# Kernel tuning notes

Hardware: AMD Instinct MI355X
Metric: run time of the kernel (lower is better)

## Reference

```python
import jax, jax.numpy as jnp
import numpy as np

POWERS = (0, 1, 2)
IN_F, OUT_F = 64, 64
B, N, T = 8, 2048, 12


def setup_inputs() -> dict:
    key = jax.random.key(0)
    ks = jax.random.split(key, 8)
    inp = {
        "x": jax.random.normal(ks[0], (B, IN_F, N, T), dtype=jnp.float32),
        "adj": jax.random.uniform(ks[1], (B, N, N), dtype=jnp.float32),
    }
    # Xavier-uniform weights per adjacency power, zero biases (as in initialize_weights)
    limit = float(np.sqrt(6.0 / (IN_F + OUT_F)))
    for i, p in enumerate(POWERS):
        inp[f"W{p}"] = jax.random.uniform(ks[2 + i], (IN_F, OUT_F), jnp.float32, -limit, limit)
        inp[f"b{p}"] = jnp.zeros((OUT_F,), jnp.float32)
    return inp


def _gcn_conv(x, adj, W, b, a_power):
    # x: [B, F, N, T]; W: [F, O]; adj: [B, N, N]
    h = jnp.einsum('bfnt,fo->bont', x, W) + b[None, :, None, None]
    # repeated diffusion along node axis: h[f, n] <- sum_m adj[n, m] h[f, m]
    for _ in range(a_power):
        h = jnp.einsum('bnm,bomt->bont', adj, h)
    return jax.nn.leaky_relu(h)  # default negative_slope 0.01, same as torch


def reference(x, adj, W0, b0, W1, b1, W2, b2):
    params = {0: (W0, b0), 1: (W1, b1), 2: (W2, b2)}
    outs = [_gcn_conv(x, adj, params[p][0], params[p][1], p) for p in POWERS]
    return jnp.concatenate(outs, axis=1)  # [B, len(POWERS)*O, N, T]
```

## Files before the change

kernel.cpp:

```cpp
#include <hip/hip_runtime.h>

#define B_ 8
#define N_ 2048
#define T_ 12
#define F_ 64
#define NT 24576
#define CH 192
#define C_ 768

typedef __bf16 bf16x8 __attribute__((ext_vector_type(8)));
typedef float f32x4 __attribute__((ext_vector_type(4)));

typedef const __attribute__((address_space(1))) unsigned int as1_uint;
typedef __attribute__((address_space(3))) unsigned int as3_uint;

__device__ __forceinline__ void gload16(const void* g, void* l) {
  __builtin_amdgcn_global_load_lds((as1_uint*)g, (as3_uint*)l, 16, 0, 0);
}

__device__ __forceinline__ unsigned short f2bf(float f) {
  unsigned int u = __float_as_uint(f);
  u += 0x7FFFu + ((u >> 16) & 1u);
  return (unsigned short)(u >> 16);
}

__device__ __forceinline__ float leaky(float v) {
  return v >= 0.0f ? v : 0.01f * v;
}

__global__ __launch_bounds__(256) void convert_adj_k(const float* __restrict__ adj,
                                                     unsigned short* __restrict__ adjb) {
  size_t i = (size_t)blockIdx.x * 256 + threadIdx.x;
  const float4 v = reinterpret_cast<const float4*>(adj)[i];
  ushort4 u;
  u.x = f2bf(v.x); u.y = f2bf(v.y); u.z = f2bf(v.z); u.w = f2bf(v.w);
  reinterpret_cast<ushort4*>(adjb)[i] = u;
}

__device__ __forceinline__ void stage_wt(const float* __restrict__ W,
                                         unsigned short* Wt, int tid) {
  const int f = tid >> 2;
  const int q = tid & 3;
  const float4* row = reinterpret_cast<const float4*>(W + f * 64 + q * 16);
#pragma unroll
  for (int v4 = 0; v4 < 4; ++v4) {
    float4 v = row[v4];
    const int ob = q * 16 + v4 * 4;
    Wt[(ob + 0) * 72 + f] = f2bf(v.x);
    Wt[(ob + 1) * 72 + f] = f2bf(v.y);
    Wt[(ob + 2) * 72 + f] = f2bf(v.z);
    Wt[(ob + 3) * 72 + f] = f2bf(v.w);
  }
}

__global__ __launch_bounds__(256) void p0_k(const float* __restrict__ x,
                                            const float* __restrict__ W0,
                                            const float* __restrict__ bia0,
                                            float* __restrict__ out) {
  __shared__ unsigned short Wt[64 * 72];
  __shared__ float bias[64];
  const int tid = threadIdx.x;
  stage_wt(W0, Wt, tid);
  if (tid < 64) bias[tid] = bia0[tid];
  __syncthreads();

  const int lane = tid & 63;
  const int wave = tid >> 6;
  const int b = blockIdx.y;
  const int e = blockIdx.x * 64 + wave * 16 + (lane & 15);
  const int fgrp = (lane >> 4) * 8;
  const float* xb = x + (size_t)b * F_ * NT;

  bf16x8 xf[2];
#pragma unroll
  for (int kf = 0; kf < 2; ++kf)
#pragma unroll
    for (int j = 0; j < 8; ++j)
      xf[kf][j] = (__bf16)xb[(size_t)(fgrp + kf * 32 + j) * NT + e];

  float* outb = out + (size_t)b * CH * NT;
#pragma unroll
  for (int ob = 0; ob < 4; ++ob) {
    f32x4 acc = {};
#pragma unroll
    for (int kf = 0; kf < 2; ++kf) {
      bf16x8 af = *reinterpret_cast<const bf16x8*>(
          &Wt[(ob * 16 + (lane & 15)) * 72 + kf * 32 + fgrp]);
      acc = __builtin_amdgcn_mfma_f32_16x16x32_bf16(af, xf[kf], acc, 0, 0, 0);
    }
#pragma unroll
    for (int r = 0; r < 4; ++r) {
      const int o = ob * 16 + (lane >> 4) * 4 + r;
      outb[(size_t)o * NT + e] = leaky(acc[r] + bias[o]);
    }
  }
}

__global__ __launch_bounds__(256) void p12_k(const float* __restrict__ x,
                                             const float* __restrict__ W1,
                                             const float* __restrict__ bia1,
                                             const float* __restrict__ W2,
                                             const float* __restrict__ bia2,
                                             unsigned short* __restrict__ G1,
                                             unsigned short* __restrict__ G2) {
  __shared__ unsigned short Wt[2][64 * 72];
  __shared__ float bias[2][64];
  const int tid = threadIdx.x;
  stage_wt(W1, Wt[0], tid);
  stage_wt(W2, Wt[1], tid);
  if (tid < 64) bias[0][tid] = bia1[tid];
  else if (tid < 128) bias[1][tid - 64] = bia2[tid - 64];
  __syncthreads();

  const int lane = tid & 63;
  const int wave = tid >> 6;
  const int b = blockIdx.y;
  const int n = blockIdx.x * 16 + (lane & 15);
  const int fgrp = (lane >> 4) * 8;
  const float* xb = x + (size_t)b * F_ * NT;
  unsigned short* Gp[2] = {G1 + (size_t)b * C_ * N_, G2 + (size_t)b * C_ * N_};

#pragma unroll
  for (int it = 0; it < 3; ++it) {
    const int t = wave * 3 + it;
    const int e = n * T_ + t;

    bf16x8 xf[2];
#pragma unroll
    for (int kf = 0; kf < 2; ++kf)
#pragma unroll
      for (int j = 0; j < 8; ++j)
        xf[kf][j] = (__bf16)xb[(size_t)(fgrp + kf * 32 + j) * NT + e];

#pragma unroll
    for (int p = 0; p < 2; ++p) {
#pragma unroll
      for (int ob = 0; ob < 4; ++ob) {
        f32x4 acc = {};
#pragma unroll
        for (int kf = 0; kf < 2; ++kf) {
          bf16x8 af = *reinterpret_cast<const bf16x8*>(
              &Wt[p][(ob * 16 + (lane & 15)) * 72 + kf * 32 + fgrp]);
          acc = __builtin_amdgcn_mfma_f32_16x16x32_bf16(af, xf[kf], acc, 0, 0, 0);
        }
#pragma unroll
        for (int r = 0; r < 4; ++r) {
          const int o = ob * 16 + (lane >> 4) * 4 + r;
          Gp[p][(size_t)(o * T_ + t) * N_ + n] = f2bf(acc[r] + bias[p][o]);
        }
      }
    }
  }
}

__global__ __launch_bounds__(512, 2) void gemm8_k(
    const unsigned short* __restrict__ adjb,
    const unsigned short* __restrict__ Bt,
    float* __restrict__ out,
    unsigned short* __restrict__ Ht,
    const int mode, const int ochan_base)
{
  extern __shared__ __align__(16) unsigned short lds[];

  const int tid  = threadIdx.x;
  const int lane = tid & 63;
  const int wave = tid >> 6;
  const int wr = wave >> 2;
  const int wc = wave & 3;

  const int b  = blockIdx.x & 7;
  const int w  = blockIdx.x >> 3;
  const int n0 = (w & 7) * 256;
  const int c0 = (w >> 3) * 192;

  const unsigned short* A  = adjb + (size_t)b * N_ * N_;
  const unsigned short* Bm = Bt   + (size_t)b * C_ * N_;

  const int swzSrc = ((lane & 3) ^ ((lane >> 3) & 3)) * 8;
  const unsigned short* aSt1 = A + (size_t)(n0 + wave * 16 + (lane >> 2)) * N_ + swzSrc;
  const unsigned short* aSt2 = aSt1 + (size_t)128 * N_;
  const unsigned short* bSt1 = Bm + (size_t)(c0 + wave * 16 + (lane >> 2)) * N_ + swzSrc;
  const int brow2 = c0 + 128 + wave * 16 + (lane >> 2);
  const unsigned short* bSt2 = Bm + (size_t)(brow2 < C_ ? brow2 : C_ - 1) * N_ + swzSrc;
  const int ldsW = wave * 512;

  const int kg  = (lane >> 4) ^ ((lane >> 1) & 3);
  const int aRd = (wr * 128 + (lane & 15)) * 32 + kg * 8;
  const int bRd = (wc * 48  + (lane & 15)) * 32 + kg * 8;

  f32x4 acc[8][3] = {};
  bf16x8 afr[8], bfr[3];

#define STGA(LDSB, KT, KH) \
  gload16(aSt1 + (KT) * 64 + (KH) * 32, lds + (LDSB) + (KH) * 8192 + ldsW); \
  gload16(aSt2 + (KT) * 64 + (KH) * 32, lds + (LDSB) + (KH) * 8192 + ldsW + 4096);

#define STGB(LDSB, KT, KH) \
  gload16(bSt1 + (KT) * 64 + (KH) * 32, lds + (LDSB) + (KH) * 8192 + ldsW); \
  gload16(bSt2 + (KT) * 64 + (KH) * 32, lds + (LDSB) + (KH) * 8192 + ldsW + 4096);

#define RD_B(BUFB, KH) { \
  _Pragma("unroll") \
  for (int nf = 0; nf < 3; ++nf) \
    bfr[nf] = *(const bf16x8*)(lds + (BUFB) + (KH) * 8192 + nf * 512 + bRd); }

#define RD_A8(BUFA, KH) { \
  _Pragma("unroll") \
  for (int mm = 0; mm < 8; ++mm) \
    afr[mm] = *(const bf16x8*)(lds + (BUFA) + (KH) * 8192 + mm * 512 + aRd); }

#define MFMA24() { \
  _Pragma("unroll") \
  for (int mm = 0; mm < 8; ++mm) \
  _Pragma("unroll") \
  for (int nf = 0; nf < 3; ++nf) \
    acc[mm][nf] = __builtin_amdgcn_mfma_f32_16x16x32_bf16( \
        afr[mm], bfr[nf], acc[mm][nf], 0, 0, 0); }

#define MIDBAR() \
  __builtin_amdgcn_s_barrier(); \
  __builtin_amdgcn_s_setprio(1);

#define ENDBAR() \
  __builtin_amdgcn_s_setprio(0); \
  __builtin_amdgcn_s_barrier();

#define WAITV_(N) asm volatile("s_waitcnt vmcnt(" #N ")" ::: "memory");
#define WAITV(N) WAITV_(N)

  STGA(0, 0, 0)      STGB(32768, 0, 0)
  STGA(0, 0, 1)      STGB(32768, 0, 1)
  STGA(16384, 1, 0)  STGB(49152, 1, 0)
  WAITV(8)
  __builtin_amdgcn_s_barrier();

#pragma unroll 1
  for (int it = 0; it < 15; ++it) {
    const int kt0 = 2 * it;
    RD_B(32768, 0) RD_A8(0, 0)
    STGA(16384, kt0 + 1, 1) STGB(49152, kt0 + 1, 1)
    WAITV(8)
    MIDBAR() MFMA24() ENDBAR()
    RD_B(32768, 1) RD_A8(0, 1)
    STGA(0, kt0 + 2, 0) STGB(32768, kt0 + 2, 0)
    WAITV(8)
    MIDBAR() MFMA24() ENDBAR()
    RD_B(49152, 0) RD_A8(16384, 0)
    STGA(0, kt0 + 2, 1) STGB(32768, kt0 + 2, 1)
    WAITV(8)
    MIDBAR() MFMA24() ENDBAR()
    RD_B(49152, 1) RD_A8(16384, 1)
    STGA(16384, kt0 + 3, 0) STGB(49152, kt0 + 3, 0)
    WAITV(8)
    MIDBAR() MFMA24() ENDBAR()
  }

  {
    RD_B(32768, 0) RD_A8(0, 0)
    STGA(16384, 31, 1) STGB(49152, 31, 1)
    WAITV(8)
    MIDBAR() MFMA24() ENDBAR()
    RD_B(32768, 1) RD_A8(0, 1)
    WAITV(4)
    MIDBAR() MFMA24() ENDBAR()
    RD_B(49152, 0) RD_A8(16384, 0)
    WAITV(0)
    MIDBAR() MFMA24() ENDBAR()
    RD_B(49152, 1) RD_A8(16384, 1)
    MIDBAR() MFMA24()
    __builtin_amdgcn_s_setprio(0);
  }

  const int r4 = (lane >> 4) * 4;
  if (mode == 0) {
    float* outb = out + (size_t)b * CH * NT;
#pragma unroll
    for (int m = 0; m < 8; ++m) {
#pragma unroll
      for (int nf = 0; nf < 3; ++nf) {
        const int c = c0 + wc * 48 + nf * 16 + (lane & 15);
        const int o = c / 12;
        const int t = c - o * 12;
#pragma unroll
        for (int r = 0; r < 4; ++r) {
          const int n = n0 + wr * 128 + m * 16 + r4 + r;
          outb[((size_t)(ochan_base + o) * N_ + n) * T_ + t] = leaky(acc[m][nf][r]);
        }
      }
    }
  } else {
    unsigned short* Hb = Ht + (size_t)b * C_ * N_;
#pragma unroll
    for (int m = 0; m < 8; ++m) {
#pragma unroll
      for (int nf = 0; nf < 3; ++nf) {
        const int c = c0 + wc * 48 + nf * 16 + (lane & 15);
        const int nb = n0 + wr * 128 + m * 16 + r4;
        ushort4 u;
        u.x = f2bf(acc[m][nf][0]);
        u.y = f2bf(acc[m][nf][1]);
        u.z = f2bf(acc[m][nf][2]);
        u.w = f2bf(acc[m][nf][3]);
        *reinterpret_cast<ushort4*>(&Hb[(size_t)c * N_ + nb]) = u;
      }
    }
  }
#undef STGA
#undef STGB
#undef RD_B
#undef RD_A8
#undef MFMA24
#undef MIDBAR
#undef ENDBAR
#undef WAITV
#undef WAITV_
}

extern "C" void kernel_launch(void* const* d_in, const int* in_sizes, int n_in,
                              void* d_out, int out_size, void* d_ws, size_t ws_size,
                              hipStream_t stream) {
  const float* x   = (const float*)d_in[0];
  const float* adj = (const float*)d_in[1];
  const float* W0  = (const float*)d_in[2];
  const float* b0  = (const float*)d_in[3];
  const float* W1  = (const float*)d_in[4];
  const float* b1  = (const float*)d_in[5];
  const float* W2  = (const float*)d_in[6];
  const float* b2  = (const float*)d_in[7];
  float* out = (float*)d_out;

  char* ws = (char*)d_ws;
  unsigned short* adjb = (unsigned short*)ws;
  unsigned short* G1   = (unsigned short*)(ws + 67108864);
  unsigned short* G2   = (unsigned short*)(ws + 92274688);
  unsigned short* Ht   = G1;

  hipFuncSetAttribute((const void*)gemm8_k,
                      hipFuncAttributeMaxDynamicSharedMemorySize, 131072);

  hipLaunchKernelGGL(convert_adj_k, dim3((B_ * N_ * N_ / 4) / 256), dim3(256), 0, stream,
                     adj, adjb);

  hipLaunchKernelGGL(p0_k, dim3(NT / 64, B_), dim3(256), 0, stream,
                     x, W0, b0, out);

  hipLaunchKernelGGL(p12_k, dim3(N_ / 16, B_), dim3(256), 0, stream,
                     x, W1, b1, W2, b2, G1, G2);

  hipLaunchKernelGGL(gemm8_k, dim3(256), dim3(512), 131072, stream,
                     adjb, G1, out, (unsigned short*)nullptr, 0, 64);

  hipLaunchKernelGGL(gemm8_k, dim3(256), dim3(512), 131072, stream,
                     adjb, G2, out, Ht, 1, 0);

  hipLaunchKernelGGL(gemm8_k, dim3(256), dim3(512), 131072, stream,
                     adjb, Ht, out, (unsigned short*)nullptr, 0, 128);
}
```

Baseline: 289.3 us.

## Add smaller-tile triple-buffered GEMM kernel for final adjacency diffusion passes

```diff
diff --git a/kernel.cpp b/kernel.cpp
--- a/kernel.cpp
+++ b/kernel.cpp
@@ -153,6 +153,118 @@
   }
 }
 
+#define TSLOT 20480
+
+__global__ __launch_bounds__(512, 2) void gemmT_k(
+    const unsigned short* __restrict__ adjb,
+    const unsigned short* __restrict__ Bt,
+    float* __restrict__ out,
+    const int ochan_base)
+{
+  extern __shared__ __align__(16) unsigned short lds[];
+
+  const int tid  = threadIdx.x;
+  const int lane = tid & 63;
+  const int wave = tid >> 6;
+  const int wr = wave >> 2;
+  const int wc = wave & 3;
+
+  const int b  = blockIdx.x & 7;
+  const int j  = blockIdx.x >> 3;
+  const int n0 = (j & 15) * 128;
+  const int c0 = (j >> 4) * 192;
+
+  const unsigned short* A  = adjb + (size_t)b * N_ * N_;
+  const unsigned short* Bm = Bt   + (size_t)b * C_ * N_;
+
+  const int swz = ((lane & 7) ^ (lane >> 3)) * 8;
+  const unsigned short* aSt = A + (size_t)(n0 + wave * 16 + (lane >> 3)) * N_ + swz;
+  const unsigned short* bSt = Bm + (size_t)(c0 + wave * 24 + (lane >> 3)) * N_ + swz;
+
+  const int lr15 = lane & 15;
+  const int x7   = lane & 7;
+  const int aBase = (wr * 64 + lr15) * 64;
+  const int bBase = 8192 + (wc * 48 + lr15) * 64;
+
+  f32x4 acc[4][3] = {};
+
+#define STG(S, KT) \
+  gload16(aSt + (KT) * 64,             lds + (S) * TSLOT + wave * 1024); \
+  gload16(aSt + 8 * N_ + (KT) * 64,    lds + (S) * TSLOT + wave * 1024 + 512); \
+  gload16(bSt + (KT) * 64,             lds + (S) * TSLOT + 8192 + wave * 1536); \
+  gload16(bSt + 8 * N_ + (KT) * 64,    lds + (S) * TSLOT + 8192 + wave * 1536 + 512); \
+  gload16(bSt + 16 * N_ + (KT) * 64,   lds + (S) * TSLOT + 8192 + wave * 1536 + 1024);
+
+#define COMP(S) { \
+  _Pragma("unroll") \
+  for (int kk = 0; kk < 2; ++kk) { \
+    const int go = ((kk * 4 + (lane >> 4)) ^ x7) * 8; \
+    bf16x8 af[4], bfv[3]; \
+    _Pragma("unroll") \
+    for (int m = 0; m < 4; ++m) \
+      af[m] = *(const bf16x8*)(lds + (S) * TSLOT + aBase + m * 1024 + go); \
+    _Pragma("unroll") \
+    for (int nf = 0; nf < 3; ++nf) \
+      bfv[nf] = *(const bf16x8*)(lds + (S) * TSLOT + bBase + nf * 1024 + go); \
+    _Pragma("unroll") \
+    for (int m = 0; m < 4; ++m) \
+    _Pragma("unroll") \
+    for (int nf = 0; nf < 3; ++nf) \
+      acc[m][nf] = __builtin_amdgcn_mfma_f32_16x16x32_bf16( \
+          af[m], bfv[nf], acc[m][nf], 0, 0, 0); \
+  } }
+
+#define WAITV_(N) asm volatile("s_waitcnt vmcnt(" #N ")" ::: "memory");
+#define WAITV(N) WAITV_(N)
+
+#define PHASE(SC, SS, KT) \
+  STG(SS, KT) \
+  WAITV(5) \
+  __builtin_amdgcn_s_barrier(); \
+  __builtin_amdgcn_s_setprio(1); \
+  COMP(SC) \
+  __builtin_amdgcn_s_setprio(0);
+
+  STG(0, 0)
+  WAITV(0)
+  __builtin_amdgcn_s_barrier();
+
+#pragma unroll 1
+  for (int t = 0; t < 30; t += 3) {
+    PHASE(0, 1, t + 1)
+    PHASE(1, 2, t + 2)
+    PHASE(2, 0, t + 3)
+  }
+  PHASE(0, 1, 31)
+  WAITV(0)
+  __builtin_amdgcn_s_barrier();
+  __builtin_amdgcn_s_setprio(1);
+  COMP(1)
+  __builtin_amdgcn_s_setprio(0);
+
+  const int r4 = (lane >> 4) * 4;
+  float* outb = out + (size_t)b * CH * NT;
+#pragma unroll
+  for (int m = 0; m < 4; ++m) {
+#pragma unroll
+    for (int nf = 0; nf < 3; ++nf) {
+      const int c = c0 + wc * 48 + nf * 16 + lr15;
+      const int o = c / 12;
+      const int t = c - o * 12;
+#pragma unroll
+      for (int r = 0; r < 4; ++r) {
+        const int n = n0 + wr * 64 + m * 16 + r4 + r;
+        outb[((size_t)(ochan_base + o) * N_ + n) * T_ + t] = leaky(acc[m][nf][r]);
+      }
+    }
+  }
+#undef STG
+#undef COMP
+#undef PHASE
+#undef WAITV
+#undef WAITV_
+}
+
 __global__ __launch_bounds__(512, 2) void gemm8_k(
     const unsigned short* __restrict__ adjb,
     const unsigned short* __restrict__ Bt,
@@ -337,6 +449,8 @@
 
   hipFuncSetAttribute((const void*)gemm8_k,
                       hipFuncAttributeMaxDynamicSharedMemorySize, 131072);
+  hipFuncSetAttribute((const void*)gemmT_k,
+                      hipFuncAttributeMaxDynamicSharedMemorySize, 122880);
 
   hipLaunchKernelGGL(convert_adj_k, dim3((B_ * N_ * N_ / 4) / 256), dim3(256), 0, stream,
                      adj, adjb);
@@ -347,12 +461,12 @@
   hipLaunchKernelGGL(p12_k, dim3(N_ / 16, B_), dim3(256), 0, stream,
                      x, W1, b1, W2, b2, G1, G2);
 
-  hipLaunchKernelGGL(gemm8_k, dim3(256), dim3(512), 131072, stream,
-                     adjb, G1, out, (unsigned short*)nullptr, 0, 64);
+  hipLaunchKernelGGL(gemmT_k, dim3(512), dim3(512), 122880, stream,
+                     adjb, G1, out, 64);
 
   hipLaunchKernelGGL(gemm8_k, dim3(256), dim3(512), 131072, stream,
                      adjb, G2, out, Ht, 1, 0);
 
-  hipLaunchKernelGGL(gemm8_k, dim3(256), dim3(512), 131072, stream,
-                     adjb, Ht, out, (unsigned short*)nullptr, 0, 128);
-}
+  hipLaunchKernelGGL(gemmT_k, dim3(512), dim3(512), 122880, stream,
+                     adjb, Ht, out, 128);
+}
```

Result: faster. 280.2 us (-3.1%).

## Diffuse raw features first and share adjacency products across powers

Applied to the files above, without the earlier changes.

```diff
diff --git a/kernel.cpp b/kernel.cpp
--- a/kernel.cpp
+++ b/kernel.cpp
@@ -24,17 +24,87 @@
   return (unsigned short)(u >> 16);
 }
 
+__device__ __forceinline__ float bf2f(unsigned short u) {
+  return __uint_as_float(((unsigned int)u) << 16);
+}
+
 __device__ __forceinline__ float leaky(float v) {
   return v >= 0.0f ? v : 0.01f * v;
 }
 
-__global__ __launch_bounds__(256) void convert_adj_k(const float* __restrict__ adj,
-                                                     unsigned short* __restrict__ adjb) {
-  size_t i = (size_t)blockIdx.x * 256 + threadIdx.x;
-  const float4 v = reinterpret_cast<const float4*>(adj)[i];
-  ushort4 u;
-  u.x = f2bf(v.x); u.y = f2bf(v.y); u.z = f2bf(v.z); u.w = f2bf(v.w);
-  reinterpret_cast<ushort4*>(adjb)[i] = u;
+__global__ __launch_bounds__(256) void convert_rs_k(const float* __restrict__ adj,
+                                                    unsigned short* __restrict__ adjb,
+                                                    float* __restrict__ rs1) {
+  const int row = blockIdx.x;
+  const int tid = threadIdx.x;
+  const int lane = tid & 63;
+  const int wave = tid >> 6;
+  const float4* src = reinterpret_cast<const float4*>(adj + (size_t)row * N_);
+  ushort4* dst = reinterpret_cast<ushort4*>(adjb + (size_t)row * N_);
+
+  float s = 0.0f;
+#pragma unroll
+  for (int i = tid; i < 512; i += 256) {
+    const float4 v = src[i];
+    ushort4 u;
+    u.x = f2bf(v.x); u.y = f2bf(v.y); u.z = f2bf(v.z); u.w = f2bf(v.w);
+    dst[i] = u;
+    s += v.x + v.y + v.z + v.w;
+  }
+#pragma unroll
+  for (int o = 32; o; o >>= 1) s += __shfl_xor(s, o);
+  __shared__ float red[4];
+  if (lane == 0) red[wave] = s;
+  __syncthreads();
+  if (tid == 0) rs1[row] = red[0] + red[1] + red[2] + red[3];
+}
+
+__global__ __launch_bounds__(256) void rs2_k(const unsigned short* __restrict__ adjb,
+                                             const float* __restrict__ rs1,
+                                             float* __restrict__ rs2) {
+  const int row = blockIdx.x;
+  const int b = row >> 11;
+  const int tid = threadIdx.x;
+  const int lane = tid & 63;
+  const int wave = tid >> 6;
+  const ushort4* src = reinterpret_cast<const ushort4*>(adjb + (size_t)row * N_);
+  const float* r1 = rs1 + ((size_t)b << 11);
+
+  float s = 0.0f;
+#pragma unroll
+  for (int i = tid; i < 512; i += 256) {
+    const ushort4 a = src[i];
+    const int m = i * 4;
+    s += bf2f(a.x) * r1[m] + bf2f(a.y) * r1[m + 1]
+       + bf2f(a.z) * r1[m + 2] + bf2f(a.w) * r1[m + 3];
+  }
+#pragma unroll
+  for (int o = 32; o; o >>= 1) s += __shfl_xor(s, o);
+  __shared__ float red[4];
+  if (lane == 0) red[wave] = s;
+  __syncthreads();
+  if (tid == 0) rs2[row] = red[0] + red[1] + red[2] + red[3];
+}
+
+__global__ __launch_bounds__(256) void convertX_k(const float* __restrict__ x,
+                                                  unsigned short* __restrict__ Xt) {
+  __shared__ float xl[T_][260];
+  const int tid = threadIdx.x;
+  const int n0 = blockIdx.x * 256;
+  const int f = blockIdx.y;
+  const int b = blockIdx.z;
+
+  const float* src = x + (((size_t)b * F_ + f) * N_ + n0 + tid) * T_;
+  float4 v0 = *reinterpret_cast<const float4*>(src);
+  float4 v1 = *reinterpret_cast<const float4*>(src + 4);
+  float4 v2 = *reinterpret_cast<const float4*>(src + 8);
+  xl[0][tid] = v0.x;  xl[1][tid] = v0.y;  xl[2][tid] = v0.z;  xl[3][tid] = v0.w;
+  xl[4][tid] = v1.x;  xl[5][tid] = v1.y;  xl[6][tid] = v1.z;  xl[7][tid] = v1.w;
+  xl[8][tid] = v2.x;  xl[9][tid] = v2.y;  xl[10][tid] = v2.z; xl[11][tid] = v2.w;
+  __syncthreads();
+#pragma unroll
+  for (int t = 0; t < T_; ++t)
+    Xt[((size_t)b * C_ + f * T_ + t) * N_ + n0 + tid] = f2bf(xl[t][tid]);
 }
 
 __device__ __forceinline__ void stage_wt(const float* __restrict__ W,
@@ -96,20 +166,17 @@
   }
 }
 
-__global__ __launch_bounds__(256) void p12_k(const float* __restrict__ x,
-                                             const float* __restrict__ W1,
-                                             const float* __restrict__ bia1,
-                                             const float* __restrict__ W2,
-                                             const float* __restrict__ bia2,
-                                             unsigned short* __restrict__ G1,
-                                             unsigned short* __restrict__ G2) {
-  __shared__ unsigned short Wt[2][64 * 72];
-  __shared__ float bias[2][64];
+__global__ __launch_bounds__(256) void pT_k(const unsigned short* __restrict__ Yt,
+                                            const float* __restrict__ W,
+                                            const float* __restrict__ bia,
+                                            const float* __restrict__ rs,
+                                            float* __restrict__ out,
+                                            const int ocb) {
+  __shared__ unsigned short Wt[64 * 72];
+  __shared__ float bias[64];
   const int tid = threadIdx.x;
-  stage_wt(W1, Wt[0], tid);
-  stage_wt(W2, Wt[1], tid);
-  if (tid < 64) bias[0][tid] = bia1[tid];
-  else if (tid < 128) bias[1][tid - 64] = bia2[tid - 64];
+  stage_wt(W, Wt, tid);
+  if (tid < 64) bias[tid] = bia[tid];
   __syncthreads();
 
   const int lane = tid & 63;
@@ -117,37 +184,34 @@
   const int b = blockIdx.y;
   const int n = blockIdx.x * 16 + (lane & 15);
   const int fgrp = (lane >> 4) * 8;
-  const float* xb = x + (size_t)b * F_ * NT;
-  unsigned short* Gp[2] = {G1 + (size_t)b * C_ * N_, G2 + (size_t)b * C_ * N_};
+  const __bf16* Yb = reinterpret_cast<const __bf16*>(Yt + (size_t)b * C_ * N_);
+  const float rsv = rs[((size_t)b << 11) + n];
+  float* outb = out + (size_t)b * CH * NT;
 
 #pragma unroll
   for (int it = 0; it < 3; ++it) {
     const int t = wave * 3 + it;
-    const int e = n * T_ + t;
 
     bf16x8 xf[2];
 #pragma unroll
     for (int kf = 0; kf < 2; ++kf)
 #pragma unroll
       for (int j = 0; j < 8; ++j)
-        xf[kf][j] = (__bf16)xb[(size_t)(fgrp + kf * 32 + j) * NT + e];
-
-#pragma unroll
-    for (int p = 0; p < 2; ++p) {
-#pragma unroll
-      for (int ob = 0; ob < 4; ++ob) {
-        f32x4 acc = {};
-#pragma unroll
-        for (int kf = 0; kf < 2; ++kf) {
-          bf16x8 af = *reinterpret_cast<const bf16x8*>(
-              &Wt[p][(ob * 16 + (lane & 15)) * 72 + kf * 32 + fgrp]);
-          acc = __builtin_amdgcn_mfma_f32_16x16x32_bf16(af, xf[kf], acc, 0, 0, 0);
-        }
-#pragma unroll
-        for (int r = 0; r < 4; ++r) {
-          const int o = ob * 16 + (lane >> 4) * 4 + r;
-          Gp[p][(size_t)(o * T_ + t) * N_ + n] = f2bf(acc[r] + bias[p][o]);
-        }
+        xf[kf][j] = Yb[(size_t)((kf * 32 + fgrp + j) * T_ + t) * N_ + n];
+
+#pragma unroll
+    for (int ob = 0; ob < 4; ++ob) {
+      f32x4 acc = {};
+#pragma unroll
+      for (int kf = 0; kf < 2; ++kf) {
+        bf16x8 af = *reinterpret_cast<const bf16x8*>(
+            &Wt[(ob * 16 + (lane & 15)) * 72 + kf * 32 + fgrp]);
+        acc = __builtin_amdgcn_mfma_f32_16x16x32_bf16(af, xf[kf], acc, 0, 0, 0);
+      }
+#pragma unroll
+      for (int r = 0; r < 4; ++r) {
+        const int o = ob * 16 + (lane >> 4) * 4 + r;
+        outb[(size_t)(ocb + o) * NT + n * T_ + t] = leaky(acc[r] + rsv * bias[o]);
       }
     }
   }
@@ -331,28 +395,35 @@
 
   char* ws = (char*)d_ws;
   unsigned short* adjb = (unsigned short*)ws;
-  unsigned short* G1   = (unsigned short*)(ws + 67108864);
-  unsigned short* G2   = (unsigned short*)(ws + 92274688);
-  unsigned short* Ht   = G1;
+  unsigned short* R1   = (unsigned short*)(ws + 67108864);
+  unsigned short* R2   = (unsigned short*)(ws + 92274688);
+  float* rs1 = (float*)(ws + 117440512);
+  float* rs2 = (float*)(ws + 117506048);
 
   hipFuncSetAttribute((const void*)gemm8_k,
                       hipFuncAttributeMaxDynamicSharedMemorySize, 131072);
 
-  hipLaunchKernelGGL(convert_adj_k, dim3((B_ * N_ * N_ / 4) / 256), dim3(256), 0, stream,
-                     adj, adjb);
+  hipLaunchKernelGGL(convert_rs_k, dim3(B_ * N_), dim3(256), 0, stream,
+                     adj, adjb, rs1);
+
+  hipLaunchKernelGGL(convertX_k, dim3(N_ / 256, F_, B_), dim3(256), 0, stream,
+                     x, R1);
 
   hipLaunchKernelGGL(p0_k, dim3(NT / 64, B_), dim3(256), 0, stream,
                      x, W0, b0, out);
 
-  hipLaunchKernelGGL(p12_k, dim3(N_ / 16, B_), dim3(256), 0, stream,
-                     x, W1, b1, W2, b2, G1, G2);
-
   hipLaunchKernelGGL(gemm8_k, dim3(256), dim3(512), 131072, stream,
-                     adjb, G1, out, (unsigned short*)nullptr, 0, 64);
+                     adjb, R1, out, R2, 1, 0);
+
+  hipLaunchKernelGGL(rs2_k, dim3(B_ * N_), dim3(256), 0, stream,
+                     adjb, rs1, rs2);
+
+  hipLaunchKernelGGL(pT_k, dim3(N_ / 16, B_), dim3(256), 0, stream,
+                     R2, W1, b1, rs1, out, 64);
 
   hipLaunchKernelGGL(gemm8_k, dim3(256), dim3(512), 131072, stream,
-                     adjb, G2, out, Ht, 1, 0);
-
-  hipLaunchKernelGGL(gemm8_k, dim3(256), dim3(512), 131072, stream,
-                     adjb, Ht, out, (unsigned short*)nullptr, 0, 128);
-}
+                     adjb, R2, out, R1, 1, 0);
+
+  hipLaunchKernelGGL(pT_k, dim3(N_ / 16, B_), dim3(256), 0, stream,
+                     R1, W2, b2, rs2, out, 128);
+}
```

Result: faster. 268.8 us (-7.1%).
